# Kernel tuning notes

Hardware: AMD Instinct MI355X
Metric: run time of the kernel (lower is better)

Reference implementation:

```python
import jax, jax.numpy as jnp
import numpy as np

N_NODES, N_RELS, N_EDGES, D = 50000, 500, 800000, 128
ALPHA = 0.2  # LeakyReLU negative slope
EPS = 1e-12


def setup_inputs() -> dict:
    key = jax.random.key(0)
    ks = jax.random.split(key, 7)
    ent = jax.random.normal(ks[0], (N_NODES, D), jnp.float32)
    rel = jax.random.normal(ks[1], (N_RELS, D), jnp.float32)
    edge_list = jax.random.randint(ks[2], (2, N_EDGES), 0, N_NODES, dtype=jnp.int64)
    rel_list = jax.random.randint(ks[3], (N_EDGES,), 0, N_RELS, dtype=jnp.int64)
    # learned params (xavier-uniform-scale normal init)
    a = jax.random.normal(ks[4], (D, 3 * D), jnp.float32) * (2.0 / (D + 3 * D)) ** 0.5
    a_2 = jax.random.normal(ks[5], (D,), jnp.float32) * (2.0 / (D + 1)) ** 0.5
    W_r = jax.random.normal(ks[6], (D, D), jnp.float32) * (2.0 / (2 * D)) ** 0.5
    return dict(ent_embedding=ent, rel_embedding=rel, edge_list=edge_list,
                rel_list=rel_list, a=a, a_2=a_2, W_r=W_r)


def reference(ent_embedding, rel_embedding, edge_list, rel_list, a, a_2, W_r):
    ent, rel = ent_embedding, rel_embedding
    N, d = ent.shape
    row, col = edge_list[0], edge_list[1]  # messages aggregated onto `row`
    a_src, a_dst, a_rel = a[:, :d], a[:, d:2 * d], a[:, 2 * d:]
    # edge message: a @ [h_src; h_dst; h_rel]  -> [E, d]  (avoid materializing the concat)
    edge_m = ent[row] @ a_src.T + ent[col] @ a_dst.T + rel[rel_list] @ a_rel.T
    powers = -jax.nn.leaky_relu(edge_m @ a_2, ALPHA)   # [E]
    edge_e = jnp.exp(powers)                           # unnormalized attention (as in KBGAT)
    e_rowsum = jax.ops.segment_sum(edge_e, row, num_segments=N)            # [N]
    h_num = jax.ops.segment_sum(edge_e[:, None] * edge_m, row, num_segments=N)  # [N, d]
    h_prime = h_num / (e_rowsum[:, None] + EPS)
    # concat=True -> ELU; SpGAT then applies dropout (identity in eval) + ReLU
    out_ent = jax.nn.relu(jax.nn.elu(h_prime))
    out_rel = jax.nn.relu(rel @ W_r) + rel
    return out_ent, out_rel
```

## Files before the change

### kernel.cpp

```cpp
#include <hip/hip_runtime.h>
#include <hip/hip_bf16.h>

#define N_NODES 50000
#define N_RELS  500
#define N_EDGES 800000
#define DIM     128
#define BUCKET  64

typedef __attribute__((ext_vector_type(8))) short bf16x8;
typedef __attribute__((ext_vector_type(4))) float f32x4;

static __device__ __forceinline__ short f2bf(float x) {
    __hip_bfloat16 h = __float2bfloat16(x);
    return *reinterpret_cast<short*>(&h);
}
static __device__ __forceinline__ float bf2f(short h) {
    return __uint_as_float(((unsigned)(unsigned short)h) << 16);
}
static __device__ __forceinline__ void split_bf(float x, short& h, short& l) {
    h = f2bf(x);
    l = f2bf(x - bf2f(h));
}

__global__ void build_Bt(const float* __restrict__ a,
                         short* __restrict__ BtH, short* __restrict__ BtL) {
    int t = blockIdx.x * 256 + threadIdx.x;
    int j = t >> 7, k = t & 127;
    const float v = (j < 128) ? a[j * 384 + k] : a[(j - 128) * 384 + 128 + k];
    short h, l;
    split_bf(v, h, l);
    BtH[t] = h;
    BtL[t] = l;
}

__global__ __launch_bounds__(256) void proj_kernel(const float* __restrict__ ent,
                                                   const short* __restrict__ BtH,
                                                   const short* __restrict__ BtL,
                                                   const float* __restrict__ a2,
                                                   float* __restrict__ projS,
                                                   __hip_bfloat16* __restrict__ projD,
                                                   float* __restrict__ sdot,
                                                   float* __restrict__ ddot) {
    const int wave = threadIdx.x >> 6;
    const int lane = threadIdx.x & 63;
    const int m    = lane & 15;
    const int quad = lane >> 4;
    const int node0 = blockIdx.x * 16;
    const int cbase = wave * 64;

    const float* arow = ent + (size_t)(node0 + m) * DIM + quad * 8;
    bf16x8 afH[4], afL[4];
#pragma unroll
    for (int kt = 0; kt < 4; kt++) {
        const float4 lo = *(const float4*)(arow + kt * 32);
        const float4 hi = *(const float4*)(arow + kt * 32 + 4);
        float xs[8] = {lo.x, lo.y, lo.z, lo.w, hi.x, hi.y, hi.z, hi.w};
        short hh[8], ll[8];
#pragma unroll
        for (int q = 0; q < 8; q++) split_bf(xs[q], hh[q], ll[q]);
        afH[kt] = (bf16x8){hh[0], hh[1], hh[2], hh[3], hh[4], hh[5], hh[6], hh[7]};
        afL[kt] = (bf16x8){ll[0], ll[1], ll[2], ll[3], ll[4], ll[5], ll[6], ll[7]};
    }

    f32x4 acc[4];
#pragma unroll
    for (int nt = 0; nt < 4; nt++) acc[nt] = (f32x4){0.f, 0.f, 0.f, 0.f};

#pragma unroll
    for (int kt = 0; kt < 4; kt++) {
        bf16x8 bH[4], bL[4];
#pragma unroll
        for (int nt = 0; nt < 4; nt++) {
            const size_t off = (size_t)(cbase + nt * 16 + m) * DIM + kt * 32 + quad * 8;
            bH[nt] = *(const bf16x8*)(BtH + off);
            bL[nt] = *(const bf16x8*)(BtL + off);
        }
#pragma unroll
        for (int nt = 0; nt < 4; nt++)
            acc[nt] = __builtin_amdgcn_mfma_f32_16x16x32_bf16(afH[kt], bH[nt], acc[nt], 0, 0, 0);
#pragma unroll
        for (int nt = 0; nt < 4; nt++)
            acc[nt] = __builtin_amdgcn_mfma_f32_16x16x32_bf16(afH[kt], bL[nt], acc[nt], 0, 0, 0);
#pragma unroll
        for (int nt = 0; nt < 4; nt++)
            acc[nt] = __builtin_amdgcn_mfma_f32_16x16x32_bf16(afL[kt], bH[nt], acc[nt], 0, 0, 0);
    }

    float part[4] = {0.f, 0.f, 0.f, 0.f};
#pragma unroll
    for (int nt = 0; nt < 4; nt++) {
        const int gc = cbase + nt * 16 + m;
        const float aw = a2[gc & 127];
#pragma unroll
        for (int reg = 0; reg < 4; reg++) {
            const int nd = node0 + quad * 4 + reg;
            const float v = acc[nt][reg];
            if (cbase < 128) projS[(size_t)nd * DIM + gc] = v;
            else             projD[(size_t)nd * DIM + (gc - 128)] = __float2bfloat16(v);
            part[reg] = fmaf(aw, v, part[reg]);
        }
    }
#pragma unroll
    for (int reg = 0; reg < 4; reg++) {
#pragma unroll
        for (int msk = 8; msk >= 1; msk >>= 1) part[reg] += __shfl_xor(part[reg], msk, 64);
    }
    __shared__ float red[4][16];
    if (m == 0) {
#pragma unroll
        for (int reg = 0; reg < 4; reg++) red[wave][quad * 4 + reg] = part[reg];
    }
    __syncthreads();
    const int t = threadIdx.x;
    if (t < 16)       sdot[node0 + t]        = red[0][t] + red[1][t];
    else if (t < 32)  ddot[node0 + (t - 16)] = red[2][t - 16] + red[3][t - 16];
}

__global__ __launch_bounds__(128) void rel_kernel(const float* __restrict__ rel,
                                                  const float* __restrict__ a,
                                                  const float* __restrict__ Wr,
                                                  const float* __restrict__ a2,
                                                  float* __restrict__ rel_proj,
                                                  float* __restrict__ rdot,
                                                  float* __restrict__ out_rel) {
    __shared__ float sR[DIM];
    __shared__ float rp[2];
    const int r = blockIdx.x, i = threadIdx.x;
    sR[i] = rel[r * DIM + i];
    __syncthreads();
    float acc1 = 0.f, acc2 = 0.f;
    const float* arow = a + i * 384 + 256;
#pragma unroll 4
    for (int k = 0; k < DIM; k++) {
        acc1 = fmaf(sR[k], arow[k], acc1);
        acc2 = fmaf(sR[k], Wr[k * DIM + i], acc2);
    }
    rel_proj[r * DIM + i] = acc1;
    out_rel[r * DIM + i] = fmaxf(acc2, 0.f) + sR[i];

    float v = acc1 * a2[i];
#pragma unroll
    for (int m = 32; m >= 1; m >>= 1) v += __shfl_xor(v, m, 64);
    if ((i & 63) == 0) rp[i >> 6] = v;
    __syncthreads();
    if (i == 0) rdot[r] = rp[0] + rp[1];
}

__global__ __launch_bounds__(256) void scatter_kernel(const int* __restrict__ edges,
                                                      const int* __restrict__ rels,
                                                      const float* __restrict__ sdot,
                                                      const float* __restrict__ ddot,
                                                      const float* __restrict__ rdot,
                                                      int* __restrict__ count,
                                                      int2* __restrict__ edat2) {
    const int e = blockIdx.x * 256 + threadIdx.x;
    if (e < N_EDGES) {
        const int row = edges[e];
        const int col = edges[N_EDGES + e];
        const int rid = rels[e];
        const float p = sdot[row] + ddot[col] + rdot[rid];
        const float pw = (p > 0.f) ? -p : -0.2f * p;
        const float ev = __expf(pw);
        const int pos = atomicAdd(&count[row], 1);
        if (pos < BUCKET)
            edat2[(size_t)row * BUCKET + pos] = make_int2(col | (rid << 16),
                                                          __float_as_int(ev));
    }
}

__global__ __launch_bounds__(256) void gather_kernel(const int* __restrict__ count,
                                                     const int2* __restrict__ edat2,
                                                     const unsigned short* __restrict__ projD,
                                                     const float* __restrict__ relp,
                                                     float* __restrict__ out) {
    const int wave = threadIdx.x >> 6;
    const int lane = threadIdx.x & 63;
    const int n = blockIdx.x * 4 + wave;
    if (n >= N_NODES) return;

    const int cnt = min(count[n], BUCKET);
    const int2 c = edat2[(size_t)n * BUCKET + lane];
    const int half = lane >> 5;
    const int d = (lane & 31) * 4;

    float4 acc = make_float4(0.f, 0.f, 0.f, 0.f);
    float esum = 0.f;
    for (int j = 0; j < cnt; j += 8) {
        int   pk[4];
        float ek[4];
#pragma unroll
        for (int k = 0; k < 4; k++) {
            const int idx = j + 2 * k + half;
            const bool val = idx < cnt;
            pk[k] = val ? __shfl(c.x, idx, 64) : 0;
            ek[k] = val ? __int_as_float(__shfl(c.y, idx, 64)) : 0.f;
        }
        uint2  uk[4];
        float4 rk[4];
#pragma unroll
        for (int k = 0; k < 4; k++) {
            uk[k] = *(const uint2*)(projD + (((size_t)(pk[k] & 0xFFFF)) << 7) + d);
            rk[k] = *(const float4*)(relp + ((pk[k] >> 16) << 7) + d);
        }
#pragma unroll
        for (int k = 0; k < 4; k++) {
            acc.x = fmaf(ek[k], __uint_as_float(uk[k].x << 16)         + rk[k].x, acc.x);
            acc.y = fmaf(ek[k], __uint_as_float(uk[k].x & 0xFFFF0000u) + rk[k].y, acc.y);
            acc.z = fmaf(ek[k], __uint_as_float(uk[k].y << 16)         + rk[k].z, acc.z);
            acc.w = fmaf(ek[k], __uint_as_float(uk[k].y & 0xFFFF0000u) + rk[k].w, acc.w);
            esum += ek[k];
        }
    }
    esum  += __shfl_xor(esum, 32, 64);
    acc.x += __shfl_xor(acc.x, 32, 64);
    acc.y += __shfl_xor(acc.y, 32, 64);
    acc.z += __shfl_xor(acc.z, 32, 64);
    acc.w += __shfl_xor(acc.w, 32, 64);

    if (half == 0) {
        const float inv = 1.f / (esum + 1e-12f);
        float* op = out + ((size_t)n << 7) + d;
        const float4 sp = *(const float4*)op;
        float4 o;
        o.x = fmaxf(fmaf(sp.x, esum, acc.x) * inv, 0.f);
        o.y = fmaxf(fmaf(sp.y, esum, acc.y) * inv, 0.f);
        o.z = fmaxf(fmaf(sp.z, esum, acc.z) * inv, 0.f);
        o.w = fmaxf(fmaf(sp.w, esum, acc.w) * inv, 0.f);
        *(float4*)op = o;
    }
}

extern "C" void kernel_launch(void* const* d_in, const int* in_sizes, int n_in,
                              void* d_out, int out_size, void* d_ws, size_t ws_size,
                              hipStream_t stream) {
    const float* ent  = (const float*)d_in[0];
    const float* rel  = (const float*)d_in[1];
    const int*   edges = (const int*)d_in[2];
    const int*   rels  = (const int*)d_in[3];
    const float* a    = (const float*)d_in[4];
    const float* a2   = (const float*)d_in[5];
    const float* Wr   = (const float*)d_in[6];

    float* out_ent = (float*)d_out;
    float* out_rel = (float*)d_out + N_NODES * DIM;

    float* relp  = (float*)d_ws;
    float* sdot  = relp + N_RELS * DIM;
    float* ddot  = sdot + N_NODES;
    float* rdot  = ddot + N_NODES;
    short* BtH   = (short*)(rdot + 512);
    short* BtL   = BtH + 256 * 128;
    unsigned short* projD = (unsigned short*)(BtL + 256 * 128);
    int2*  edat2 = (int2*)(projD + (size_t)N_NODES * DIM);
    int*   count = (int*)(edat2 + (size_t)N_NODES * BUCKET);

    hipMemsetAsync(count, 0, N_NODES * sizeof(int), stream);

    build_Bt<<<128, 256, 0, stream>>>(a, BtH, BtL);
    proj_kernel<<<N_NODES / 16, 256, 0, stream>>>(ent, BtH, BtL, a2, out_ent,
                                                  (__hip_bfloat16*)projD, sdot, ddot);
    rel_kernel<<<N_RELS, 128, 0, stream>>>(rel, a, Wr, a2, relp, rdot, out_rel);

    scatter_kernel<<<(N_EDGES + 255) / 256, 256, 0, stream>>>(edges, rels, sdot, ddot,
                                                              rdot, count, edat2);

    gather_kernel<<<(N_NODES + 3) / 4, 256, 0, stream>>>(count, edat2, projD, relp,
                                                         out_ent);
}
```

Measured before the change: 254.2 us.

## Stage projection weights in LDS via direct global-to-LDS loads and retile proj_kernel

After: 212.5 us (median of 2 runs). -16.4%, faster.

```diff
diff --git a/kernel.cpp b/kernel.cpp
--- a/kernel.cpp
+++ b/kernel.cpp
@@ -21,99 +21,120 @@
     h = f2bf(x);
     l = f2bf(x - bf2f(h));
 }
-
-__global__ void build_Bt(const float* __restrict__ a,
-                         short* __restrict__ BtH, short* __restrict__ BtL) {
-    int t = blockIdx.x * 256 + threadIdx.x;
-    int j = t >> 7, k = t & 127;
+static __device__ __forceinline__ void gload_lds16(const void* g, void* s) {
+    __builtin_amdgcn_global_load_lds(
+        (const __attribute__((address_space(1))) char*)g,
+        (__attribute__((address_space(3))) char*)s, 16, 0, 0);
+}
+
+__global__ void build_Bt(const float* __restrict__ a, short* __restrict__ Bt2) {
+    const int t = blockIdx.x * 256 + threadIdx.x;
+    const int q    = t & 7;
+    const int lane = (t >> 3) & 63;
+    const int f    = (t >> 9) & 15;
+    const int hl   = (t >> 13) & 1;
+    const int cg   = t >> 14;
+    const int ct = f & 3, kt = f >> 2;
+    const int j = cg * 64 + ct * 16 + (lane & 15);
+    const int k = kt * 32 + (lane >> 4) * 8 + q;
     const float v = (j < 128) ? a[j * 384 + k] : a[(j - 128) * 384 + 128 + k];
     short h, l;
     split_bf(v, h, l);
-    BtH[t] = h;
-    BtL[t] = l;
+    Bt2[t] = hl ? l : h;
 }
 
 __global__ __launch_bounds__(256) void proj_kernel(const float* __restrict__ ent,
-                                                   const short* __restrict__ BtH,
-                                                   const short* __restrict__ BtL,
+                                                   const short* __restrict__ Bt2,
                                                    const float* __restrict__ a2,
                                                    float* __restrict__ projS,
-                                                   __hip_bfloat16* __restrict__ projD,
+                                                   unsigned short* __restrict__ projD,
                                                    float* __restrict__ sdot,
                                                    float* __restrict__ ddot) {
+    const int cg   = blockIdx.x & 3;
+    const int nb   = blockIdx.x >> 2;
     const int wave = threadIdx.x >> 6;
     const int lane = threadIdx.x & 63;
     const int m    = lane & 15;
     const int quad = lane >> 4;
-    const int node0 = blockIdx.x * 16;
-    const int cbase = wave * 64;
-
-    const float* arow = ent + (size_t)(node0 + m) * DIM + quad * 8;
+    const int node0 = nb * 64 + wave * 16;
+
+    __shared__ short sB[16384];
+
+    {
+        const char* gbase = (const char*)(Bt2 + cg * 16384);
+        char* sbase = (char*)sB;
+#pragma unroll
+        for (int i = 0; i < 8; i++) {
+            const int region = (wave * 8 + i) * 1024;
+            gload_lds16(gbase + region + lane * 16, sbase + region);
+        }
+    }
+
+    const bool active = (node0 < N_NODES);
+
     bf16x8 afH[4], afL[4];
+    if (active) {
+        const float* arow = ent + (size_t)(node0 + m) * DIM + quad * 8;
+#pragma unroll
+        for (int kt = 0; kt < 4; kt++) {
+            const float4 lo = *(const float4*)(arow + kt * 32);
+            const float4 hi = *(const float4*)(arow + kt * 32 + 4);
+            float xs[8] = {lo.x, lo.y, lo.z, lo.w, hi.x, hi.y, hi.z, hi.w};
+            short hh[8], ll[8];
+#pragma unroll
+            for (int q = 0; q < 8; q++) split_bf(xs[q], hh[q], ll[q]);
+            afH[kt] = (bf16x8){hh[0], hh[1], hh[2], hh[3], hh[4], hh[5], hh[6], hh[7]};
+            afL[kt] = (bf16x8){ll[0], ll[1], ll[2], ll[3], ll[4], ll[5], ll[6], ll[7]};
+        }
+    }
+
+    __syncthreads();
+    if (!active) return;
+
+    f32x4 acc[4];
+#pragma unroll
+    for (int ct = 0; ct < 4; ct++) acc[ct] = (f32x4){0.f, 0.f, 0.f, 0.f};
+
 #pragma unroll
     for (int kt = 0; kt < 4; kt++) {
-        const float4 lo = *(const float4*)(arow + kt * 32);
-        const float4 hi = *(const float4*)(arow + kt * 32 + 4);
-        float xs[8] = {lo.x, lo.y, lo.z, lo.w, hi.x, hi.y, hi.z, hi.w};
-        short hh[8], ll[8];
-#pragma unroll
-        for (int q = 0; q < 8; q++) split_bf(xs[q], hh[q], ll[q]);
-        afH[kt] = (bf16x8){hh[0], hh[1], hh[2], hh[3], hh[4], hh[5], hh[6], hh[7]};
-        afL[kt] = (bf16x8){ll[0], ll[1], ll[2], ll[3], ll[4], ll[5], ll[6], ll[7]};
-    }
-
-    f32x4 acc[4];
-#pragma unroll
-    for (int nt = 0; nt < 4; nt++) acc[nt] = (f32x4){0.f, 0.f, 0.f, 0.f};
-
-#pragma unroll
-    for (int kt = 0; kt < 4; kt++) {
-        bf16x8 bH[4], bL[4];
-#pragma unroll
-        for (int nt = 0; nt < 4; nt++) {
-            const size_t off = (size_t)(cbase + nt * 16 + m) * DIM + kt * 32 + quad * 8;
-            bH[nt] = *(const bf16x8*)(BtH + off);
-            bL[nt] = *(const bf16x8*)(BtL + off);
-        }
-#pragma unroll
-        for (int nt = 0; nt < 4; nt++)
-            acc[nt] = __builtin_amdgcn_mfma_f32_16x16x32_bf16(afH[kt], bH[nt], acc[nt], 0, 0, 0);
-#pragma unroll
-        for (int nt = 0; nt < 4; nt++)
-            acc[nt] = __builtin_amdgcn_mfma_f32_16x16x32_bf16(afH[kt], bL[nt], acc[nt], 0, 0, 0);
-#pragma unroll
-        for (int nt = 0; nt < 4; nt++)
-            acc[nt] = __builtin_amdgcn_mfma_f32_16x16x32_bf16(afL[kt], bH[nt], acc[nt], 0, 0, 0);
-    }
-
-    float part[4] = {0.f, 0.f, 0.f, 0.f};
-#pragma unroll
-    for (int nt = 0; nt < 4; nt++) {
-        const int gc = cbase + nt * 16 + m;
-        const float aw = a2[gc & 127];
-#pragma unroll
-        for (int reg = 0; reg < 4; reg++) {
-            const int nd = node0 + quad * 4 + reg;
-            const float v = acc[nt][reg];
-            if (cbase < 128) projS[(size_t)nd * DIM + gc] = v;
-            else             projD[(size_t)nd * DIM + (gc - 128)] = __float2bfloat16(v);
-            part[reg] = fmaf(aw, v, part[reg]);
-        }
-    }
-#pragma unroll
-    for (int reg = 0; reg < 4; reg++) {
-#pragma unroll
-        for (int msk = 8; msk >= 1; msk >>= 1) part[reg] += __shfl_xor(part[reg], msk, 64);
-    }
-    __shared__ float red[4][16];
-    if (m == 0) {
-#pragma unroll
-        for (int reg = 0; reg < 4; reg++) red[wave][quad * 4 + reg] = part[reg];
-    }
-    __syncthreads();
-    const int t = threadIdx.x;
-    if (t < 16)       sdot[node0 + t]        = red[0][t] + red[1][t];
-    else if (t < 32)  ddot[node0 + (t - 16)] = red[2][t - 16] + red[3][t - 16];
+#pragma unroll
+        for (int ct = 0; ct < 4; ct++) {
+            const int f = kt * 4 + ct;
+            const bf16x8 bH = *(const bf16x8*)(sB + f * 512 + lane * 8);
+            const bf16x8 bL = *(const bf16x8*)(sB + 8192 + f * 512 + lane * 8);
+            acc[ct] = __builtin_amdgcn_mfma_f32_16x16x32_bf16(bH, afH[kt], acc[ct], 0, 0, 0);
+            acc[ct] = __builtin_amdgcn_mfma_f32_16x16x32_bf16(bL, afH[kt], acc[ct], 0, 0, 0);
+            acc[ct] = __builtin_amdgcn_mfma_f32_16x16x32_bf16(bH, afL[kt], acc[ct], 0, 0, 0);
+        }
+    }
+
+    float part = 0.f;
+    const int colbase = (cg & 1) * 64;
+#pragma unroll
+    for (int ct = 0; ct < 4; ct++) {
+        const int coff = colbase + ct * 16 + quad * 4;
+        const float4 aw = *(const float4*)(a2 + coff);
+        part = fmaf(aw.x, acc[ct][0], part);
+        part = fmaf(aw.y, acc[ct][1], part);
+        part = fmaf(aw.z, acc[ct][2], part);
+        part = fmaf(aw.w, acc[ct][3], part);
+        const size_t off = (size_t)(node0 + m) * DIM + coff;
+        if (cg < 2) {
+            *(float4*)(projS + off) = make_float4(acc[ct][0], acc[ct][1],
+                                                  acc[ct][2], acc[ct][3]);
+        } else {
+            ushort4 u;
+            u.x = (unsigned short)f2bf(acc[ct][0]);
+            u.y = (unsigned short)f2bf(acc[ct][1]);
+            u.z = (unsigned short)f2bf(acc[ct][2]);
+            u.w = (unsigned short)f2bf(acc[ct][3]);
+            *(ushort4*)(projD + off) = u;
+        }
+    }
+    part += __shfl_xor(part, 16, 64);
+    part += __shfl_xor(part, 32, 64);
+    if (quad == 0)
+        atomicAdd(((cg < 2) ? sdot : ddot) + node0 + m, part);
 }
 
 __global__ __launch_bounds__(128) void rel_kernel(const float* __restrict__ rel,
@@ -179,7 +200,8 @@
     if (n >= N_NODES) return;
 
     const int cnt = min(count[n], BUCKET);
-    const int2 c = edat2[(size_t)n * BUCKET + lane];
+    int2 c = make_int2(0, 0);
+    if (lane < cnt) c = edat2[(size_t)n * BUCKET + lane];
     const int half = lane >> 5;
     const int d = (lane & 31) * 4;
 
@@ -248,17 +270,19 @@
     float* sdot  = relp + N_RELS * DIM;
     float* ddot  = sdot + N_NODES;
     float* rdot  = ddot + N_NODES;
-    short* BtH   = (short*)(rdot + 512);
-    short* BtL   = BtH + 256 * 128;
-    unsigned short* projD = (unsigned short*)(BtL + 256 * 128);
+    short* Bt2   = (short*)(rdot + 512);
+    unsigned short* projD = (unsigned short*)(Bt2 + 65536);
     int2*  edat2 = (int2*)(projD + (size_t)N_NODES * DIM);
     int*   count = (int*)(edat2 + (size_t)N_NODES * BUCKET);
 
     hipMemsetAsync(count, 0, N_NODES * sizeof(int), stream);
-
-    build_Bt<<<128, 256, 0, stream>>>(a, BtH, BtL);
-    proj_kernel<<<N_NODES / 16, 256, 0, stream>>>(ent, BtH, BtL, a2, out_ent,
-                                                  (__hip_bfloat16*)projD, sdot, ddot);
+    hipMemsetAsync(sdot, 0, 2 * N_NODES * sizeof(float), stream);
+
+    build_Bt<<<256, 256, 0, stream>>>(a, Bt2);
+
+    const int NB = (N_NODES + 63) / 64;
+    proj_kernel<<<NB * 4, 256, 0, stream>>>(ent, Bt2, a2, out_ent, projD, sdot, ddot);
+
     rel_kernel<<<N_RELS, 128, 0, stream>>>(rel, a, Wr, a2, relp, rdot, out_rel);
 
     scatter_kernel<<<(N_EDGES + 255) / 256, 256, 0, stream>>>(edges, rels, sdot, ddot,
```
